# Kernel optimization log

Measured on AMD Instinct MI355X. Metric: run time of the kernel, lower is better.

The kernel has to match this reference:

```python
import jax, jax.numpy as jnp
import numpy as np
import math

B, H, S, D = 2, 16, 2048, 64

def setup_inputs() -> dict:
    key = jax.random.key(0)
    kq, kk, kv = jax.random.split(key, 3)
    Q = jax.random.normal(kq, (B, H, S, D), dtype=jnp.float32)
    K = jax.random.normal(kk, (B, H, S, D), dtype=jnp.float32)
    V = jax.random.normal(kv, (B, H, S, D), dtype=jnp.float32)
    causal_mask = jnp.tril(jnp.ones((S, S), dtype=bool))
    return {"Q": Q, "K": K, "V": V, "causal_mask": causal_mask}

def reference(Q, K, V, causal_mask):
    d_k = K.shape[-1]
    scores = jnp.einsum('bhqd,bhkd->bhqk', Q, K) / math.sqrt(d_k)
    scores = jnp.where(causal_mask, scores, -jnp.inf)
    probs = jax.nn.softmax(scores, axis=-1)
    return jnp.einsum('bhqk,bhkd->bhqd', probs, V)
```

## Files before the change

### kernel.cpp

```cpp
#include <hip/hip_runtime.h>
#include <math.h>


constexpr int kS   = 2048;
constexpr int kD   = 64;
constexpr int kBH  = 32;
constexpr int kPadP = 72;
constexpr int kFragBH = 64 * 4 * 512;

typedef short short8 __attribute__((ext_vector_type(8)));
typedef float float4v __attribute__((ext_vector_type(4)));
typedef float float16v __attribute__((ext_vector_type(16)));
typedef unsigned int u32;
typedef unsigned short u16;

static __device__ inline u16 f2bf(float f) {
  union { float f; unsigned u; } v; v.f = f;
  unsigned r = v.u + 0x7FFF + ((v.u >> 16) & 1);
  return (u16)(r >> 16);
}

static __device__ inline short8 pack8(float4v a, float4v b) {
  short8 r;
  r[0] = (short)f2bf(a[0]); r[1] = (short)f2bf(a[1]);
  r[2] = (short)f2bf(a[2]); r[3] = (short)f2bf(a[3]);
  r[4] = (short)f2bf(b[0]); r[5] = (short)f2bf(b[1]);
  r[6] = (short)f2bf(b[2]); r[7] = (short)f2bf(b[3]);
  return r;
}

static __device__ inline void swap32(u32 a, u32 b, u32& oa, u32& ob) {
#if __has_builtin(__builtin_amdgcn_permlane32_swap)
  auto r = __builtin_amdgcn_permlane32_swap(a, b, false, false);
  oa = r[0]; ob = r[1];
#else
  asm volatile("v_permlane32_swap_b32 %0, %1" : "+v"(a), "+v"(b));
  oa = a; ob = b;
#endif
}

__global__ __launch_bounds__(256)
void prep_kernel(const float* __restrict__ K, const float* __restrict__ V,
                 u16* __restrict__ Kf, u16* __restrict__ Vf) {
  __shared__ u16 tile[64 * kPadP];
  const int tid = threadIdx.x;
  const int bh = blockIdx.y, st = blockIdx.x;
  const size_t ibase = (size_t)bh * kS * kD + (size_t)st * 64 * kD;
  const size_t fbase = (size_t)bh * kFragBH;
  const int r  = tid >> 2;
  const int c0 = (tid & 3) * 16;
  const int dk = tid & 3;
  const int U  = st * 2 + (r >> 5);
  const int lr = r & 31;
  {
    const float* kp = K + ibase + (size_t)r * kD + c0;
    float4v a = *(const float4v*)(kp);
    float4v b = *(const float4v*)(kp + 4);
    float4v c = *(const float4v*)(kp + 8);
    float4v d = *(const float4v*)(kp + 12);
    u16* dst = Kf + fbase + (size_t)(U * 4 + dk) * 512;
    *(short8*)(dst + lr * 8)        = pack8(a, b);
    *(short8*)(dst + (32 + lr) * 8) = pack8(c, d);
  }
  {
    const float* vp = V + ibase + (size_t)r * kD + c0;
    float4v a = *(const float4v*)(vp);
    float4v b = *(const float4v*)(vp + 4);
    float4v c = *(const float4v*)(vp + 8);
    float4v d = *(const float4v*)(vp + 12);
    u16* t = &tile[r * kPadP + c0];
    *(short8*)t       = pack8(a, b);
    *(short8*)(t + 8) = pack8(c, d);
  }
  __syncthreads();
  {
    const int dd = tid >> 2;
    const int s0 = (tid & 3) * 16;
    short8 w0, w1;
    #pragma unroll
    for (int i = 0; i < 8; ++i) {
      w0[i] = (short)tile[(s0 + i) * kPadP + dd];
      w1[i] = (short)tile[(s0 + 8 + i) * kPadP + dd];
    }
    const int ku   = st * 2 + (s0 >> 5);
    const int koff = s0 & 31;
    const int c    = ((koff >> 4) << 1) | (dd >> 5);
    u16* vdst = Vf + fbase + (size_t)(ku * 4 + c) * 512;
    *(short8*)(vdst + (dd & 31) * 8)        = w0;
    *(short8*)(vdst + (32 + (dd & 31)) * 8) = w1;
  }
}

__global__ __launch_bounds__(256, 3)
void fattn_kernel(const float* __restrict__ Qp, const u16* __restrict__ Kf,
                  const u16* __restrict__ Vf, float* __restrict__ O) {
  __shared__ u32   ldsP[5][32][33];
  __shared__ float ldsL[5][32];

  const int tid  = threadIdx.x;
  const int wave = tid >> 6;
  const int lane = tid & 63;
  const int l31  = lane & 31;
  const int h    = lane >> 5;

  const int blk = blockIdx.x;
  const int bh  = (blk & 7) * 4 + ((blk >> 3) & 3);
  const int sA  = blk >> 5;
  const int sB  = 63 - sA;
  const int t   = sB + 1;
  const int lo  = (65 * wave) >> 2;
  const int hi  = (65 * (wave + 1)) >> 2;
  const int uT  = min(max(t, lo), hi);

  const u16* gk = Kf + (size_t)bh * kFragBH + lane * 8;
  const u16* gv = Vf + (size_t)bh * kFragBH + lane * 8;

  float16v zf;
  #pragma unroll
  for (int i = 0; i < 16; ++i) zf[i] = 0.f;

  float16v acc0 = zf, acc1 = zf;
  float lac = 0.f;
  short8 qf[4];

  auto loadQ = [&](int s) {
    const float scl = 0.125f * 1.44269504089f;
    const float* qp = Qp + ((size_t)bh * kS + (size_t)(s * 32 + l31)) * kD + h * 8;
    #pragma unroll
    for (int dk = 0; dk < 4; ++dk) {
      float4v a = *(const float4v*)(qp + dk * 16);
      float4v b = *(const float4v*)(qp + dk * 16 + 4);
      #pragma unroll
      for (int i = 0; i < 4; ++i) { a[i] *= scl; b[i] *= scl; }
      qf[dk] = pack8(a, b);
    }
  };

  auto unitCompute = [&](int k, int sdiag) {
    const u16* kp = gk + (size_t)k * 2048;
    const u16* vp = gv + (size_t)k * 2048;
    short8 kf[4], vf[4];
    #pragma unroll
    for (int i = 0; i < 4; ++i) kf[i] = *(const short8*)(kp + i * 512);
    #pragma unroll
    for (int i = 0; i < 4; ++i) vf[i] = *(const short8*)(vp + i * 512);

    __builtin_amdgcn_s_setprio(1);
    float16v sv = __builtin_amdgcn_mfma_f32_32x32x16_bf16(kf[0], qf[0], zf, 0, 0, 0);
    sv = __builtin_amdgcn_mfma_f32_32x32x16_bf16(kf[1], qf[1], sv, 0, 0, 0);
    sv = __builtin_amdgcn_mfma_f32_32x32x16_bf16(kf[2], qf[2], sv, 0, 0, 0);
    sv = __builtin_amdgcn_mfma_f32_32x32x16_bf16(kf[3], qf[3], sv, 0, 0, 0);
    __builtin_amdgcn_s_setprio(0);

    if (k == sdiag) {
      const int qg = sdiag * 32 + l31;
      #pragma unroll
      for (int r = 0; r < 16; ++r) {
        const int kg = k * 32 + (r & 3) + 8 * (r >> 2) + 4 * h;
        if (kg > qg) sv[r] = -1e30f;
      }
    }

    u32 pk[8];
    #pragma unroll
    for (int g2 = 0; g2 < 4; ++g2) {
      const u32 u0 = __float_as_uint(__builtin_amdgcn_exp2f(sv[4 * g2 + 0]));
      const u32 u1 = __float_as_uint(__builtin_amdgcn_exp2f(sv[4 * g2 + 1]));
      const u32 u2 = __float_as_uint(__builtin_amdgcn_exp2f(sv[4 * g2 + 2]));
      const u32 u3 = __float_as_uint(__builtin_amdgcn_exp2f(sv[4 * g2 + 3]));
      pk[2 * g2]     = __builtin_amdgcn_perm(u1, u0, 0x07060302u);
      pk[2 * g2 + 1] = __builtin_amdgcn_perm(u3, u2, 0x07060302u);
    }

    {
      float e0 = 0.f, e1 = 0.f;
      #pragma unroll
      for (int i = 0; i < 4; ++i) {
        e0 += __uint_as_float(pk[i] << 16)     + __uint_as_float(pk[i] & 0xFFFF0000u);
        e1 += __uint_as_float(pk[i + 4] << 16) + __uint_as_float(pk[i + 4] & 0xFFFF0000u);
      }
      lac += e0 + e1;
    }

    union { u32 u[4]; short8 s8; } pf;
    swap32(pk[0], pk[2], pf.u[0], pf.u[2]);
    swap32(pk[1], pk[3], pf.u[1], pf.u[3]);
    __builtin_amdgcn_s_setprio(1);
    acc0 = __builtin_amdgcn_mfma_f32_32x32x16_bf16(pf.s8, vf[0], acc0, 0, 0, 0);
    acc1 = __builtin_amdgcn_mfma_f32_32x32x16_bf16(pf.s8, vf[1], acc1, 0, 0, 0);
    __builtin_amdgcn_s_setprio(0);
    swap32(pk[4], pk[6], pf.u[0], pf.u[2]);
    swap32(pk[5], pk[7], pf.u[1], pf.u[3]);
    __builtin_amdgcn_s_setprio(1);
    acc0 = __builtin_amdgcn_mfma_f32_32x32x16_bf16(pf.s8, vf[2], acc0, 0, 0, 0);
    acc1 = __builtin_amdgcn_mfma_f32_32x32x16_bf16(pf.s8, vf[3], acc1, 0, 0, 0);
    __builtin_amdgcn_s_setprio(0);
  };

  auto dump = [&](int slot) {
    #pragma unroll
    for (int r = 0; r < 16; ++r) {
      const int row = (r & 3) + 8 * (r >> 2) + 4 * h;
      ldsP[slot][row][l31] = (u32)f2bf(acc0[r]) | ((u32)f2bf(acc1[r]) << 16);
    }
    const float lt = lac + __shfl_xor(lac, 32);
    if (lane < 32) ldsL[slot][lane] = lt;
  };

  if (lo < uT) {
    loadQ(sB);
    for (int u = lo; u < uT; ++u) unitCompute(u, sB);
    dump(wave);
    acc0 = zf; acc1 = zf; lac = 0.f;
  }
  if (uT < hi) {
    loadQ(sA);
    for (int u = uT; u < hi; ++u) unitCompute(u - t, sA);
    dump((lo < uT) ? 4 : wave);
  }

  __syncthreads();

  {
    const int setid = tid >> 7;
    const int sOut  = setid ? sA : sB;
    const bool v0 = setid ? (0  >= t) : (0  < t);
    const bool v1 = setid ? (16 >= t) : (16 < t);
    const bool v2 = setid ? (32 >= t) : (32 < t);
    const bool v3 = setid ? (48 >= t) : (48 < t);
    const bool v4 = (setid != 0) && (t != 48);

    const int q  = (tid & 127) >> 2;
    const int c0 = (tid & 3) * 8;

    float lsum = 0.f;
    if (v0) lsum += ldsL[0][q];
    if (v1) lsum += ldsL[1][q];
    if (v2) lsum += ldsL[2][q];
    if (v3) lsum += ldsL[3][q];
    if (v4) lsum += ldsL[4][q];
    const float inv = 1.f / lsum;

    float* op = O + ((size_t)bh * kS + sOut * 32 + q) * kD;
    #pragma unroll
    for (int i = 0; i < 8; ++i) {
      const int c = c0 + i;
      float lov = 0.f, hiv = 0.f;
      if (v0) { const u32 p = ldsP[0][q][c]; lov += __uint_as_float(p << 16); hiv += __uint_as_float(p & 0xFFFF0000u); }
      if (v1) { const u32 p = ldsP[1][q][c]; lov += __uint_as_float(p << 16); hiv += __uint_as_float(p & 0xFFFF0000u); }
      if (v2) { const u32 p = ldsP[2][q][c]; lov += __uint_as_float(p << 16); hiv += __uint_as_float(p & 0xFFFF0000u); }
      if (v3) { const u32 p = ldsP[3][q][c]; lov += __uint_as_float(p << 16); hiv += __uint_as_float(p & 0xFFFF0000u); }
      if (v4) { const u32 p = ldsP[4][q][c]; lov += __uint_as_float(p << 16); hiv += __uint_as_float(p & 0xFFFF0000u); }
      op[c]      = lov * inv;
      op[c + 32] = hiv * inv;
    }
  }
}

extern "C" void kernel_launch(void* const* d_in, const int* in_sizes, int n_in,
                              void* d_out, int out_size, void* d_ws, size_t ws_size,
                              hipStream_t stream) {
  const float* Q = (const float*)d_in[0];
  const float* K = (const float*)d_in[1];
  const float* V = (const float*)d_in[2];
  float* O = (float*)d_out;

  const size_t nKV = (size_t)kBH * kS * kD;
  u16* Kf = (u16*)d_ws;
  u16* Vf = Kf + nKV;

  dim3 gprep(kS / 64, kBH);
  prep_kernel<<<gprep, 256, 0, stream>>>(K, V, Kf, Vf);
  fattn_kernel<<<1024, 256, 0, stream>>>(Q, Kf, Vf, O);
}
```

Measured before the change: 135.9 us.

## Split each block's KV units across eight waves instead of four

Each block now runs 512 threads (8 waves), so the 65 KV units of the paired query tiles are split into eight shorter ranges instead of four. The LDS partial buffers grow from 5 to 9 slots, and the final reduction is rewritten as a loop over the wave slots, with each thread handling 4 columns. This cuts the serial KV loop length per wave and adds parallelism, at the cost of more LDS, more partial-sum reduction work, and a tighter register budget under launch_bounds(512,8).

Result: slower. 368.1 us (+170.9%).

```diff
diff --git a/kernel.cpp b/kernel.cpp
--- a/kernel.cpp
+++ b/kernel.cpp
@@ -91,11 +91,11 @@
   }
 }
 
-__global__ __launch_bounds__(256, 3)
+__global__ __launch_bounds__(512, 8)
 void fattn_kernel(const float* __restrict__ Qp, const u16* __restrict__ Kf,
                   const u16* __restrict__ Vf, float* __restrict__ O) {
-  __shared__ u32   ldsP[5][32][33];
-  __shared__ float ldsL[5][32];
+  __shared__ u32   ldsP[9][32][33];
+  __shared__ float ldsL[9][32];
 
   const int tid  = threadIdx.x;
   const int wave = tid >> 6;
@@ -108,8 +108,8 @@
   const int sA  = blk >> 5;
   const int sB  = 63 - sA;
   const int t   = sB + 1;
-  const int lo  = (65 * wave) >> 2;
-  const int hi  = (65 * (wave + 1)) >> 2;
+  const int lo  = (65 * wave) >> 3;
+  const int hi  = (65 * (wave + 1)) >> 3;
   const int uT  = min(max(t, lo), hi);
 
   const u16* gk = Kf + (size_t)bh * kFragBH + lane * 8;
@@ -216,43 +216,48 @@
   if (uT < hi) {
     loadQ(sA);
     for (int u = uT; u < hi; ++u) unitCompute(u - t, sA);
-    dump((lo < uT) ? 4 : wave);
+    dump((lo < uT) ? 8 : wave);
   }
 
   __syncthreads();
 
   {
-    const int setid = tid >> 7;
+    const int setid = tid >> 8;
     const int sOut  = setid ? sA : sB;
-    const bool v0 = setid ? (0  >= t) : (0  < t);
-    const bool v1 = setid ? (16 >= t) : (16 < t);
-    const bool v2 = setid ? (32 >= t) : (32 < t);
-    const bool v3 = setid ? (48 >= t) : (48 < t);
-    const bool v4 = (setid != 0) && (t != 48);
-
-    const int q  = (tid & 127) >> 2;
-    const int c0 = (tid & 3) * 8;
-
-    float lsum = 0.f;
-    if (v0) lsum += ldsL[0][q];
-    if (v1) lsum += ldsL[1][q];
-    if (v2) lsum += ldsL[2][q];
-    if (v3) lsum += ldsL[3][q];
-    if (v4) lsum += ldsL[4][q];
-    const float inv = 1.f / lsum;
-
+    const int q  = (tid & 255) >> 3;
+    const int c0 = (tid & 7) * 4;
+
+    float lsumv = 0.f;
+    float lov[4] = {0.f, 0.f, 0.f, 0.f}, hiv[4] = {0.f, 0.f, 0.f, 0.f};
+    #pragma unroll
+    for (int w = 0; w < 8; ++w) {
+      const int low = (65 * w) >> 3;
+      const bool val = setid ? (low >= t) : (low < t);
+      if (val) {
+        lsumv += ldsL[w][q];
+        #pragma unroll
+        for (int i = 0; i < 4; ++i) {
+          const u32 p = ldsP[w][q][c0 + i];
+          lov[i] += __uint_as_float(p << 16);
+          hiv[i] += __uint_as_float(p & 0xFFFF0000u);
+        }
+      }
+    }
+    if (setid && (t != 40) && (t != 48) && (t != 56)) {
+      lsumv += ldsL[8][q];
+      #pragma unroll
+      for (int i = 0; i < 4; ++i) {
+        const u32 p = ldsP[8][q][c0 + i];
+        lov[i] += __uint_as_float(p << 16);
+        hiv[i] += __uint_as_float(p & 0xFFFF0000u);
+      }
+    }
+    const float inv = 1.f / lsumv;
     float* op = O + ((size_t)bh * kS + sOut * 32 + q) * kD;
     #pragma unroll
-    for (int i = 0; i < 8; ++i) {
-      const int c = c0 + i;
-      float lov = 0.f, hiv = 0.f;
-      if (v0) { const u32 p = ldsP[0][q][c]; lov += __uint_as_float(p << 16); hiv += __uint_as_float(p & 0xFFFF0000u); }
-      if (v1) { const u32 p = ldsP[1][q][c]; lov += __uint_as_float(p << 16); hiv += __uint_as_float(p & 0xFFFF0000u); }
-      if (v2) { const u32 p = ldsP[2][q][c]; lov += __uint_as_float(p << 16); hiv += __uint_as_float(p & 0xFFFF0000u); }
-      if (v3) { const u32 p = ldsP[3][q][c]; lov += __uint_as_float(p << 16); hiv += __uint_as_float(p & 0xFFFF0000u); }
-      if (v4) { const u32 p = ldsP[4][q][c]; lov += __uint_as_float(p << 16); hiv += __uint_as_float(p & 0xFFFF0000u); }
-      op[c]      = lov * inv;
-      op[c + 32] = hiv * inv;
+    for (int i = 0; i < 4; ++i) {
+      op[c0 + i]      = lov[i] * inv;
+      op[c0 + i + 32] = hiv[i] * inv;
     }
   }
 }
@@ -271,5 +276,5 @@
 
   dim3 gprep(kS / 64, kBH);
   prep_kernel<<<gprep, 256, 0, stream>>>(K, V, Kf, Vf);
-  fattn_kernel<<<1024, 256, 0, stream>>>(Q, Kf, Vf, O);
-}
+  fattn_kernel<<<1024, 512, 0, stream>>>(Q, Kf, Vf, O);
+}
```
